# Kernel optimization log

Measured on AMD Instinct MI355X. Metric: run time of the kernel, lower is better.

Reference implementation:

```python
import jax, jax.numpy as jnp
import numpy as np

B, T, V, E, H, L = 128, 512, 128, 256, 1024, 2


def setup_inputs() -> dict:
    key = jax.random.key(0)
    ks = jax.random.split(key, 8)
    scale_e = 1.0 / np.sqrt(E)
    scale0 = 1.0 / np.sqrt(E + H)
    scale1 = 1.0 / np.sqrt(2 * H)
    return {
        "input_batch": jax.random.randint(ks[0], (B, T), 0, V, dtype=jnp.int32),
        "input_lengths": jax.random.randint(ks[1], (B,), 1, T + 1, dtype=jnp.int32),
        "char_embeddings": jax.random.normal(ks[2], (V, E), dtype=jnp.float32) * scale_e,
        "W0": jax.random.normal(ks[3], (E + H, 4 * H), dtype=jnp.float32) * scale0,
        "b0": jnp.zeros((4 * H,), dtype=jnp.float32),
        "W1": jax.random.normal(ks[4], (2 * H, 4 * H), dtype=jnp.float32) * scale1,
        "b1": jnp.zeros((4 * H,), dtype=jnp.float32),
    }


def _lstm_cell(x, h, c, W, b):
    # TF BasicLSTMCell: gates in order (i, j, f, o), forget_bias = 1.0
    z = jnp.concatenate([x, h], axis=-1) @ W + b  # [B, 4H]
    i, j, f, o = jnp.split(z, 4, axis=-1)
    new_c = c * jax.nn.sigmoid(f + 1.0) + jax.nn.sigmoid(i) * jnp.tanh(j)
    new_h = jnp.tanh(new_c) * jax.nn.sigmoid(o)
    return new_h, new_c


def reference(input_batch, input_lengths, char_embeddings, W0, b0, W1, b1):
    # embedding lookup: [B, T, E] -> time-major [T, B, E]
    xs = jnp.swapaxes(char_embeddings[input_batch], 0, 1)
    t_idx = jnp.arange(T, dtype=jnp.int32)
    zeros = jnp.zeros((B, H), dtype=xs.dtype)
    init = (zeros, zeros, zeros, zeros)  # (h0, c0, h1, c1)

    def step(carry, inp):
        h0, c0, h1, c1 = carry
        x_t, t = inp
        mask = (t < input_lengths)[:, None]  # [B, 1] dynamic_rnn length mask
        nh0, nc0 = _lstm_cell(x_t, h0, c0, W0, b0)
        nh0 = jnp.where(mask, nh0, h0)
        nc0 = jnp.where(mask, nc0, c0)
        nh1, nc1 = _lstm_cell(nh0, h1, c1, W1, b1)
        nh1 = jnp.where(mask, nh1, h1)
        nc1 = jnp.where(mask, nc1, c1)
        out = jnp.where(mask, nh1, 0.0)  # dynamic_rnn zeros outputs past length
        return (nh0, nc0, nh1, nc1), out

    _, outputs = jax.lax.scan(step, init, (xs, t_idx))  # outputs: [T, B, H]
    outputs_bt = jnp.swapaxes(outputs, 0, 1)  # [B, T, H]
    # reverse_sequence + slice[:, 0, :] == output at last valid timestep
    idx = (input_lengths - 1)[:, None, None]  # [B, 1, 1]
    encoder_last_output = jnp.take_along_axis(outputs_bt, idx, axis=1)[:, 0, :]
    return encoder_last_output  # [B, H]
```

## Files before the change

kernel.cpp:

```cpp
#include <hip/hip_runtime.h>


namespace {
constexpr int NBLK = 256, THREADS = 512;
constexpr int KT0B = 40;
constexpr int KT1B = 64;
constexpr int NPH = 513;
constexpr int HPS = 128 * 1024;
constexpr int SPIN_CAP = 2000000;
constexpr int F_CREG = 0;
constexpr int F_BOOT = 128;
constexpr int F_ARR  = 256;
constexpr int F_XARR = 576;
}

typedef _Float16 f16x8 __attribute__((ext_vector_type(8)));
typedef float f32x4 __attribute__((ext_vector_type(4)));
typedef unsigned u32x4 __attribute__((ext_vector_type(4)));

__host__ __device__ __forceinline__ int fswz(int kk) {
  return ((kk & 15) >> 2) * 8 + (kk >> 4) * 4 + (kk & 3);
}

__device__ __forceinline__ float sigm(float x) { return 1.0f / (1.0f + __expf(-x)); }
__device__ __forceinline__ float tanh_f(float x) {
  float e = __expf(-2.0f * fabsf(x));
  float r = (1.0f - e) / (1.0f + e);
  return x >= 0.0f ? r : -r;
}
__device__ __forceinline__ unsigned short f2h(float f) {
  _Float16 h = (_Float16)f;
  return __builtin_bit_cast(unsigned short, h);
}

__device__ __forceinline__ int load_i32_llc(const int* p) {
  int v;
  asm volatile("global_load_dword %0, %1, off sc0 sc1\n\ts_waitcnt vmcnt(0)"
               : "=v"(v) : "v"(p) : "memory");
  return v;
}
__device__ __forceinline__ uint4 llc_load_issue(const unsigned* p) {
  uint4 v;
  asm volatile("global_load_dwordx4 %0, %1, off sc0 sc1" : "=v"(v) : "v"(p));
  return v;
}
__device__ __forceinline__ void vm_wait0() {
  asm volatile("s_waitcnt vmcnt(0)" ::: "memory");
  __builtin_amdgcn_sched_barrier(0);
}
__device__ __forceinline__ void store_u32_llc(unsigned* p, unsigned v) {
  asm volatile("global_store_dword %0, %1, off sc0 sc1" :: "v"(p), "v"(v) : "memory");
}
__device__ __forceinline__ void store_u16_llc(unsigned short* p, unsigned short v) {
  asm volatile("global_store_short %0, %1, off sc0 sc1" :: "v"(p), "v"(v) : "memory");
}
__device__ __forceinline__ void inv_l1() {
  asm volatile("buffer_inv" ::: "memory");
}
__device__ __forceinline__ int xcc_id() {
  int x;
  asm("s_getreg_b32 %0, hwreg(HW_REG_XCC_ID)" : "=s"(x));
  return x & 7;
}
__device__ __forceinline__ int spin_ge(int* p, int target) {
  for (int it = 0; it < SPIN_CAP; ++it) {
    if (load_i32_llc(p) >= target) return 1;
    __builtin_amdgcn_s_sleep(1);
  }
  return 0;
}
__device__ __forceinline__ f16x8 ash(u32x4 v) { return __builtin_bit_cast(f16x8, v); }
__device__ __forceinline__ f16x8 ash4(uint4 v) { return __builtin_bit_cast(f16x8, v); }

#define MFMA1(acc, ah, bh)                                                    \
  acc = __builtin_amdgcn_mfma_f32_16x16x32_f16(ah, bh, acc, 0, 0, 0);


__global__ void prep_sort(const int* __restrict__ lens, int* __restrict__ perm,
                          int* __restrict__ lenS, int* __restrict__ ncnt) {
  __shared__ int k_[128], p_[128];
  const int tid = threadIdx.x;
  if (tid < 128) { k_[tid] = (lens[tid] << 8) | (127 - tid); p_[tid] = tid; }
  __syncthreads();
  for (int ph = 0; ph < 128; ++ph) {
    if (tid < 64) {
      int a = 2 * tid + (ph & 1), b = a + 1;
      if (b < 128 && k_[a] < k_[b]) {
        int tk = k_[a]; k_[a] = k_[b]; k_[b] = tk;
        int tp = p_[a]; p_[a] = p_[b]; p_[b] = tp;
      }
    }
    __syncthreads();
  }
  if (tid < 128) { perm[tid] = p_[tid]; lenS[tid] = k_[tid] >> 8; }
  if (tid < 512) {
    int c = 0;
    for (int i = 0; i < 128; ++i) c += ((k_[i] >> 8) > tid) ? 1 : 0;
    ncnt[tid] = c;
  }
}

__global__ void prep_emb(const float* __restrict__ emb,
                         unsigned short* __restrict__ ef) {
  int i = blockIdx.x * 256 + threadIdx.x;
  int row = i >> 8, e = i & 255;
  int pos = row * 256 + (e >> 5) * 32 + fswz(e & 31);
  ef[pos] = f2h(emb[i]);
}

__global__ void prep_wslab(const float* __restrict__ W, uint4* __restrict__ Whi,
                           int KT) {
  int e = blockIdx.x * 256 + threadIdx.x;
  int lane = e & 63;
  int kt = (e >> 6) % KT;
  int blk = e / (64 * KT);
  int cf = lane & 15;
  int g = cf & 3, ul = cf >> 2;
  int col = g * 1024 + blk * 4 + ul;
  int kbase = kt * 32 + ((lane >> 4) & 3) * 4;
  unsigned hi[8];
#pragma unroll
  for (int j = 0; j < 8; ++j) {
    int k = kbase + (j & 3) + 16 * (j >> 2);
    float f = W[(size_t)k * 4096 + col];
    hi[j] = __builtin_bit_cast(unsigned short, (_Float16)f);
  }
  uint4 vh;
  vh.x = hi[0] | (hi[1] << 16); vh.y = hi[2] | (hi[3] << 16);
  vh.z = hi[4] | (hi[5] << 16); vh.w = hi[6] | (hi[7] << 16);
  Whi[e] = vh;
}


__global__ __launch_bounds__(THREADS, 1) void lstm_persist(
    const int* __restrict__ ib,
    const float* __restrict__ bias0, const float* __restrict__ bias1,
    const uint4* __restrict__ Whi0g, const uint4* __restrict__ Whi1g,
    const unsigned short* __restrict__ embF,
    const int* __restrict__ perm, const int* __restrict__ lenS,
    const int* __restrict__ ncnt,
    unsigned short* hg0, unsigned short* hg1,
    unsigned short* rep,
    int* ctr, float* __restrict__ out) {
  const int bid = blockIdx.x;
  const int tid = threadIdx.x;
  const int w = tid >> 6;
  const int lane = tid & 63;
  const int lr = lane & 15;
  const int lg4 = ((lane >> 4) & 3) * 4;
  const int slotE = ((lane >> 4) & 3) * 8;
  const int arow = w * 16 + lr;
  const int srow = tid >> 2;
  const int cu = tid & 3;
  const int ug = bid * 4 + cu;
  const int fpos = (ug >> 5) * 32 + fswz(ug & 31);
  const int permA = perm[arow];
  const int cperm = perm[srow];
  const int clen = lenS[srow];

  __shared__ uint4 Wh0[KT0B * 64];
  __shared__ uint4 Wh1[KT1B * 64];
  __shared__ float zb[128][17];
  __shared__ int s_x, s_rk, s_R, s_ok;

  {
    const uint4* s0 = Whi0g + (size_t)bid * (KT0B * 64);
    for (int i = tid; i < KT0B * 64; i += THREADS) Wh0[i] = s0[i];
    const uint4* s1 = Whi1g + (size_t)bid * (KT1B * 64);
    for (int i = tid; i < KT1B * 64; i += THREADS) Wh1[i] = s1[i];
  }

  float bz0[4], bz1[4];
#pragma unroll
  for (int g = 0; g < 4; ++g) {
    bz0[g] = bias0[g * 1024 + ug];
    bz1[g] = bias1[g * 1024 + ug];
  }
  float c0r = 0.0f, c1r = 0.0f;

  if (tid == 0) {
    s_ok = 1;
    int x = xcc_id();
    s_x = x;
    s_rk = atomicAdd(&ctr[F_CREG + x * 16], 1);
    vm_wait0();
    atomicAdd(&ctr[F_BOOT], 1);
    if (!spin_ge(&ctr[F_BOOT], NBLK)) s_ok = 0;
    int Rv = 1;
    for (int i = 0; i < 8; ++i) {
      int r = load_i32_llc(&ctr[F_CREG + i * 16]);
      if (i == s_x) Rv = r;
    }
    s_R = Rv;
  }
  __syncthreads();
  const int xcd = s_x, rk = s_rk, R = s_R;
  if (!s_ok) return;

  unsigned short* repB = rep + (size_t)xcd * 2 * HPS;
  const unsigned short* A0 = repB + (size_t)arow * 1024;
  const unsigned short* A1 = repB + HPS + (size_t)arow * 1024;

  const int pl = tid >> 8;
  const int rowoff = (tid >> 7) & 1;
  const int ch = (tid & 127) * 8;
  unsigned short* dp = repB + pl * HPS;

  for (int p = 0; p < NPH; ++p) {
    const int nact0 = (p < 512) ? ncnt[p] : 0;
    const int nact1 = (p >= 1) ? ncnt[p - 1] : 0;
    const bool doL0 = (p < 512) && (w * 16 < nact0);
    const bool doL1 = (p >= 1) && (w * 16 < nact1);
    const int ncopy = ncnt[p == 0 ? 0 : p - 1];

    f32x4 acc0 = (f32x4){0.f, 0.f, 0.f, 0.f};
    f32x4 acc1 = (f32x4){0.f, 0.f, 0.f, 0.f};

    const unsigned short* sp =
        (pl == 0) ? (hg0 + (size_t)((p + 2) % 3) * HPS)
                  : (hg1 + (size_t)((p + 1) % 3) * HPS);
    const int step = 2 * R;
    const int dr0 = 2 * rk + rowoff;
    const int dr1 = dr0 + step, dr2 = dr0 + 2 * step, dr3 = dr0 + 3 * step;
    uint4 dv0, dv1, dv2, dv3;
    if (dr0 < ncopy) dv0 = llc_load_issue((const unsigned*)(sp + dr0 * 1024 + ch));
    if (dr1 < ncopy) dv1 = llc_load_issue((const unsigned*)(sp + dr1 * 1024 + ch));
    if (dr2 < ncopy) dv2 = llc_load_issue((const unsigned*)(sp + dr2 * 1024 + ch));
    if (dr3 < ncopy) dv3 = llc_load_issue((const unsigned*)(sp + dr3 * 1024 + ch));

    if (doL0) {
      const int tok = ib[(size_t)permA * 512 + p];
      const unsigned short* ef = embF + tok * 256;
#pragma unroll
      for (int kt = 0; kt < 8; ++kt) {
        const f16x8 ah = ash(*(const u32x4*)(ef + kt * 32 + slotE));
        MFMA1(acc0, ah, ash4(Wh0[kt * 64 + lane]))
      }
    }

    vm_wait0();
    if (dr0 < ncopy) *(uint4*)(dp + dr0 * 1024 + ch) = dv0;
    if (dr1 < ncopy) *(uint4*)(dp + dr1 * 1024 + ch) = dv1;
    if (dr2 < ncopy) *(uint4*)(dp + dr2 * 1024 + ch) = dv2;
    if (dr3 < ncopy) *(uint4*)(dp + dr3 * 1024 + ch) = dv3;
    for (int r = dr0 + 4 * step; r < ncopy; r += step) {
      uint4 v = llc_load_issue((const unsigned*)(sp + r * 1024 + ch));
      vm_wait0();
      *(uint4*)(dp + r * 1024 + ch) = v;
    }
    __syncthreads();

    if (tid == 0) store_u32_llc((unsigned*)&ctr[F_XARR + xcd * 64 + rk], p + 1);
    if (tid < 64 && tid < R) {
      if (!spin_ge(&ctr[F_XARR + xcd * 64 + tid], p + 1)) s_ok = 0;
    }
    __syncthreads();
    if (!s_ok) break;
    inv_l1();

    if (doL0 || doL1) {
#pragma unroll 8
      for (int q = 0; q < 32; ++q) {
        const f16x8 ah = ash(*(const u32x4*)(A0 + q * 32 + slotE));
        if (doL0) { MFMA1(acc0, ah, ash4(Wh0[(8 + q) * 64 + lane])) }
        if (doL1) { MFMA1(acc1, ah, ash4(Wh1[q * 64 + lane])) }
      }
    }
    if (doL1) {
#pragma unroll 8
      for (int q = 0; q < 32; ++q) {
        const f16x8 ah = ash(*(const u32x4*)(A1 + q * 32 + slotE));
        MFMA1(acc1, ah, ash4(Wh1[(32 + q) * 64 + lane]))
      }
    }

    __syncthreads();
    if (doL0) {
#pragma unroll
      for (int rr = 0; rr < 4; ++rr) zb[w * 16 + lg4 + rr][lr] = acc0[rr];
    }
    __syncthreads();
    const bool act0 = (p < 512) && (p < clen);
    float z0i = 0, z0j = 0, z0f = 0, z0o = 0;
    if (act0) {
      z0i = zb[srow][cu * 4 + 0] + bz0[0];
      z0j = zb[srow][cu * 4 + 1] + bz0[1];
      z0f = zb[srow][cu * 4 + 2] + bz0[2];
      z0o = zb[srow][cu * 4 + 3] + bz0[3];
    }
    __syncthreads();
    if (doL1) {
#pragma unroll
      for (int rr = 0; rr < 4; ++rr) zb[w * 16 + lg4 + rr][lr] = acc1[rr];
    }
    if (act0) {
      const float nc = c0r * sigm(z0f + 1.0f) + sigm(z0i) * tanh_f(z0j);
      const float nh = tanh_f(nc) * sigm(z0o);
      c0r = nc;
      store_u16_llc(&hg0[(size_t)(p % 3) * HPS + srow * 1024 + fpos], f2h(nh));
    }
    __syncthreads();
    if (p >= 1 && (p - 1) < clen) {
      const float z1i = zb[srow][cu * 4 + 0] + bz1[0];
      const float z1j = zb[srow][cu * 4 + 1] + bz1[1];
      const float z1f = zb[srow][cu * 4 + 2] + bz1[2];
      const float z1o = zb[srow][cu * 4 + 3] + bz1[3];
      const float nc = c1r * sigm(z1f + 1.0f) + sigm(z1i) * tanh_f(z1j);
      const float nh = tanh_f(nc) * sigm(z1o);
      c1r = nc;
      store_u16_llc(&hg1[(size_t)((p + 2) % 3) * HPS + srow * 1024 + fpos], f2h(nh));
      if (p - 1 == clen - 1) out[(size_t)cperm * 1024 + ug] = nh;
    }

    vm_wait0();
    __syncthreads();
    if (tid == 0) store_u32_llc((unsigned*)&ctr[F_ARR + bid], p + 1);
    if (tid < 256) {
      if (!spin_ge(&ctr[F_ARR + tid], p + 1)) s_ok = 0;
    }
    __syncthreads();
    if (!s_ok) break;
  }
}


extern "C" void kernel_launch(void* const* d_in, const int* in_sizes, int n_in,
                              void* d_out, int out_size, void* d_ws, size_t ws_size,
                              hipStream_t stream) {
  const int*   ib   = (const int*)d_in[0];
  const int*   lens = (const int*)d_in[1];
  const float* emb  = (const float*)d_in[2];
  const float* W0   = (const float*)d_in[3];
  const float* b0   = (const float*)d_in[4];
  const float* W1   = (const float*)d_in[5];
  const float* b1   = (const float*)d_in[6];
  (void)in_sizes; (void)n_in; (void)out_size; (void)ws_size;

  char* ws = (char*)d_ws;
  size_t off = 0;
  auto alloc = [&](size_t bytes) { char* q = ws + off; off += (bytes + 255) & ~(size_t)255; return q; };

  int*            ctr  = (int*)alloc(8192);
  unsigned short* hg0  = (unsigned short*)alloc((size_t)3 * HPS * 2);
  unsigned short* hg1  = (unsigned short*)alloc((size_t)3 * HPS * 2);
  const size_t zero_bytes = off;
  unsigned short* embF = (unsigned short*)alloc(128 * 256 * 2);
  int*            perm = (int*)alloc(4096);
  int*            lenS = perm + 128;
  int*            ncnt = perm + 256;
  unsigned short* rep  = (unsigned short*)alloc((size_t)8 * 2 * HPS * 2);
  uint4*          Whi0 = (uint4*)alloc((size_t)NBLK * KT0B * 64 * 16);
  uint4*          Whi1 = (uint4*)alloc((size_t)NBLK * KT1B * 64 * 16);

  hipMemsetAsync(d_ws, 0, zero_bytes, stream);
  prep_sort<<<1, 512, 0, stream>>>(lens, perm, lenS, ncnt);
  prep_emb<<<128, 256, 0, stream>>>(emb, embF);
  prep_wslab<<<(NBLK * KT0B * 64) / 256, 256, 0, stream>>>(W0, Whi0, KT0B);
  prep_wslab<<<(NBLK * KT1B * 64) / 256, 256, 0, stream>>>(W1, Whi1, KT1B);
  lstm_persist<<<NBLK, THREADS, 0, stream>>>(
      ib, b0, b1, Whi0, Whi1, embF,
      perm, lenS, ncnt, hg0, hg1, rep, ctr, (float*)d_out);
}
```

Measured before the change: 9.094 ms.

## Use hierarchical per-XCD grid barrier, double-buffer A loads, merge gate barriers

Replaces the flat 256-block grid barrier, where each block polled every other block's flag, with a two-level barrier. A leader block per XCD gathers its local blocks and publishes an XCD-done flag, and every block then polls only the 8 XCD flags. The MFMA loops now prefetch A-operand vectors in double-buffered register groups, and separate zb buffers for the two layers let several __syncthreads in the gate phase be removed. The changes cut cross-die polling traffic and barrier latency per timestep, at the cost of more registers and an extra serial hop through the leader block.

New measurement: 7.468 ms. 17.9% less time.

```diff
diff --git a/kernel.cpp b/kernel.cpp
--- a/kernel.cpp
+++ b/kernel.cpp
@@ -8,10 +8,11 @@
 constexpr int NPH = 513;
 constexpr int HPS = 128 * 1024;
 constexpr int SPIN_CAP = 2000000;
-constexpr int F_CREG = 0;
-constexpr int F_BOOT = 128;
-constexpr int F_ARR  = 256;
-constexpr int F_XARR = 576;
+constexpr int F_CREG  = 0;
+constexpr int F_BOOT  = 128;
+constexpr int F_GARR  = 256;
+constexpr int F_XDONE = 768;
+constexpr int F_XARR  = 1024;
 }
 
 typedef _Float16 f16x8 __attribute__((ext_vector_type(8)));
@@ -160,8 +161,8 @@
 
   __shared__ uint4 Wh0[KT0B * 64];
   __shared__ uint4 Wh1[KT1B * 64];
-  __shared__ float zb[128][17];
-  __shared__ int s_x, s_rk, s_R, s_ok;
+  __shared__ float zb[2][128][17];
+  __shared__ int s_x, s_rk, s_R, s_pres, s_ok;
 
   {
     const uint4* s0 = Whi0g + (size_t)bid * (KT0B * 64);
@@ -186,15 +187,17 @@
     vm_wait0();
     atomicAdd(&ctr[F_BOOT], 1);
     if (!spin_ge(&ctr[F_BOOT], NBLK)) s_ok = 0;
-    int Rv = 1;
+    int Rv = 1, pres = 0;
     for (int i = 0; i < 8; ++i) {
       int r = load_i32_llc(&ctr[F_CREG + i * 16]);
+      if (r > 0) pres |= (1 << i);
       if (i == s_x) Rv = r;
     }
     s_R = Rv;
+    s_pres = pres;
   }
   __syncthreads();
-  const int xcd = s_x, rk = s_rk, R = s_R;
+  const int xcd = s_x, rk = s_rk, R = s_R, pres = s_pres;
   if (!s_ok) return;
 
   unsigned short* repB = rep + (size_t)xcd * 2 * HPS;
@@ -259,54 +262,74 @@
     inv_l1();
 
     if (doL0 || doL1) {
-#pragma unroll 8
-      for (int q = 0; q < 32; ++q) {
-        const f16x8 ah = ash(*(const u32x4*)(A0 + q * 32 + slotE));
-        if (doL0) { MFMA1(acc0, ah, ash4(Wh0[(8 + q) * 64 + lane])) }
-        if (doL1) { MFMA1(acc1, ah, ash4(Wh1[q * 64 + lane])) }
-      }
+      u32x4 a[2][8];
+#pragma unroll
+      for (int i = 0; i < 8; ++i) a[0][i] = *(const u32x4*)(A0 + i * 32 + slotE);
+#pragma unroll
+      for (int g = 0; g < 4; ++g) {
+        const int cb = g & 1;
+        if (g < 3) {
+#pragma unroll
+          for (int i = 0; i < 8; ++i)
+            a[cb ^ 1][i] = *(const u32x4*)(A0 + ((g + 1) * 8 + i) * 32 + slotE);
+        } else if (doL1) {
+#pragma unroll
+          for (int i = 0; i < 8; ++i)
+            a[cb ^ 1][i] = *(const u32x4*)(A1 + i * 32 + slotE);
+        }
+#pragma unroll
+        for (int i = 0; i < 8; ++i) {
+          const int q = g * 8 + i;
+          const f16x8 ah = ash(a[cb][i]);
+          if (doL0) { MFMA1(acc0, ah, ash4(Wh0[(8 + q) * 64 + lane])) }
+          if (doL1) { MFMA1(acc1, ah, ash4(Wh1[q * 64 + lane])) }
+        }
+      }
+      if (doL1) {
+#pragma unroll
+        for (int g = 0; g < 4; ++g) {
+          const int cb = g & 1;
+          if (g < 3) {
+#pragma unroll
+            for (int i = 0; i < 8; ++i)
+              a[cb ^ 1][i] = *(const u32x4*)(A1 + ((g + 1) * 8 + i) * 32 + slotE);
+          }
+#pragma unroll
+          for (int i = 0; i < 8; ++i) {
+            const int q = g * 8 + i;
+            const f16x8 ah = ash(a[cb][i]);
+            MFMA1(acc1, ah, ash4(Wh1[(32 + q) * 64 + lane]))
+          }
+        }
+      }
+    }
+
+    if (doL0) {
+#pragma unroll
+      for (int rr = 0; rr < 4; ++rr) zb[0][w * 16 + lg4 + rr][lr] = acc0[rr];
     }
     if (doL1) {
-#pragma unroll 8
-      for (int q = 0; q < 32; ++q) {
-        const f16x8 ah = ash(*(const u32x4*)(A1 + q * 32 + slotE));
-        MFMA1(acc1, ah, ash4(Wh1[(32 + q) * 64 + lane]))
-      }
-    }
-
-    __syncthreads();
-    if (doL0) {
-#pragma unroll
-      for (int rr = 0; rr < 4; ++rr) zb[w * 16 + lg4 + rr][lr] = acc0[rr];
-    }
-    __syncthreads();
-    const bool act0 = (p < 512) && (p < clen);
-    float z0i = 0, z0j = 0, z0f = 0, z0o = 0;
-    if (act0) {
-      z0i = zb[srow][cu * 4 + 0] + bz0[0];
-      z0j = zb[srow][cu * 4 + 1] + bz0[1];
-      z0f = zb[srow][cu * 4 + 2] + bz0[2];
-      z0o = zb[srow][cu * 4 + 3] + bz0[3];
-    }
-    __syncthreads();
-    if (doL1) {
-#pragma unroll
-      for (int rr = 0; rr < 4; ++rr) zb[w * 16 + lg4 + rr][lr] = acc1[rr];
-    }
-    if (act0) {
-      const float nc = c0r * sigm(z0f + 1.0f) + sigm(z0i) * tanh_f(z0j);
-      const float nh = tanh_f(nc) * sigm(z0o);
+#pragma unroll
+      for (int rr = 0; rr < 4; ++rr) zb[1][w * 16 + lg4 + rr][lr] = acc1[rr];
+    }
+    __syncthreads();
+    if (p < 512 && p < clen) {
+      const float zi = zb[0][srow][cu * 4 + 0] + bz0[0];
+      const float zj = zb[0][srow][cu * 4 + 1] + bz0[1];
+      const float zf = zb[0][srow][cu * 4 + 2] + bz0[2];
+      const float zo = zb[0][srow][cu * 4 + 3] + bz0[3];
+      const float nc = c0r * sigm(zf + 1.0f) + sigm(zi) * tanh_f(zj);
+      const float nh = tanh_f(nc) * sigm(zo);
       c0r = nc;
       store_u16_llc(&hg0[(size_t)(p % 3) * HPS + srow * 1024 + fpos], f2h(nh));
     }
-    __syncthreads();
     if (p >= 1 && (p - 1) < clen) {
-      const float z1i = zb[srow][cu * 4 + 0] + bz1[0];
-      const float z1j = zb[srow][cu * 4 + 1] + bz1[1];
-      const float z1f = zb[srow][cu * 4 + 2] + bz1[2];
-      const float z1o = zb[srow][cu * 4 + 3] + bz1[3];
-      const float nc = c1r * sigm(z1f + 1.0f) + sigm(z1i) * tanh_f(z1j);
-      const float nh = tanh_f(nc) * sigm(z1o);
+      const float zi = zb[1][srow][cu * 4 + 0] + bz1[0];
+      const float zj = zb[1][srow][cu * 4 + 1] + bz1[1];
+      const float zf = zb[1][srow][cu * 4 + 2] + bz1[2];
+      const float zo = zb[1][srow][cu * 4 + 3] + bz1[3];
+      const float nc = c1r * sigm(zf + 1.0f) + sigm(zi) * tanh_f(zj);
+      const float nh = tanh_f(nc) * sigm(zo);
       c1r = nc;
       store_u16_llc(&hg1[(size_t)((p + 2) % 3) * HPS + srow * 1024 + fpos], f2h(nh));
       if (p - 1 == clen - 1) out[(size_t)cperm * 1024 + ug] = nh;
@@ -314,9 +337,16 @@
 
     vm_wait0();
     __syncthreads();
-    if (tid == 0) store_u32_llc((unsigned*)&ctr[F_ARR + bid], p + 1);
-    if (tid < 256) {
-      if (!spin_ge(&ctr[F_ARR + tid], p + 1)) s_ok = 0;
+    if (tid == 0) store_u32_llc((unsigned*)&ctr[F_GARR + xcd * 64 + rk], p + 1);
+    if (rk == 0) {
+      if (tid < 64 && tid < R) {
+        if (!spin_ge(&ctr[F_GARR + xcd * 64 + tid], p + 1)) s_ok = 0;
+      }
+      __syncthreads();
+      if (tid == 0) store_u32_llc((unsigned*)&ctr[F_XDONE + xcd * 16], p + 1);
+    }
+    if (tid < 8 && ((pres >> tid) & 1)) {
+      if (!spin_ge(&ctr[F_XDONE + tid * 16], p + 1)) s_ok = 0;
     }
     __syncthreads();
     if (!s_ok) break;
```
